# Performance work log

Measured on AMD Instinct MI355X. Metric: run time of the kernel, lower is better.

The kernel has to match this reference:

```python
import jax, jax.numpy as jnp
import numpy as np
from jax.scipy.special import logsumexp

L = 5          # label_size (fixed by label2idx)
START = 3
END = 4
PAD = 2
NEG = -10000.0


def setup_inputs() -> dict:
    B, S = 4096, 512
    key = jax.random.key(0)
    k1, k2, k3, k4 = jax.random.split(key, 4)
    lstm_scores = jax.random.normal(k1, (B, S, L), dtype=jnp.float32)
    transition = jax.random.normal(k2, (L, L), dtype=jnp.float32)
    transition = (transition.at[:, START].set(NEG)
                            .at[END, :].set(NEG)
                            .at[:, PAD].set(NEG)
                            .at[PAD, :].set(NEG))
    word_seq_lens = jax.random.randint(k3, (B,), 1, S + 1)  # lengths in [1, S]
    tags = jax.random.randint(k4, (B, S), 0, 2)             # gold labels in {0,1}
    mask = jnp.arange(S)[None, :] < word_seq_lens[:, None]   # (B, S) bool
    return {"lstm_scores": lstm_scores, "transition": transition,
            "word_seq_lens": word_seq_lens, "tags": tags, "mask": mask}


def reference(lstm_scores, transition, word_seq_lens, tags, mask):
    B, S, _ = lstm_scores.shape
    # all_scores[b,t,i,j] = transition[i,j] + emission[b,t,j]  -> (B,S,L,L)
    all_scores = transition[None, None, :, :] + lstm_scores[:, :, None, :]

    # ---- forward algorithm (normalizer) via scan over time ----
    alpha0 = all_scores[:, 0, START, :]              # (B, L)
    scores_t = jnp.swapaxes(all_scores, 0, 1)        # (S, B, L, L)

    def step(alpha, sc_t):
        new = logsumexp(alpha[:, :, None] + sc_t, axis=1)  # (B, L)
        return new, new

    _, alphas = jax.lax.scan(step, alpha0, scores_t[1:])   # (S-1, B, L)
    alphas = jnp.concatenate([alpha0[None], alphas], axis=0)  # (S, B, L)
    alphas = jnp.swapaxes(alphas, 0, 1)                       # (B, S, L)

    idx = jnp.broadcast_to((word_seq_lens - 1)[:, None, None], (B, 1, L))
    last_alpha = jnp.take_along_axis(alphas, idx, axis=1)[:, 0, :]  # (B, L)
    last_alpha = last_alpha + transition[:, END][None, :]
    unlabeled = jnp.sum(logsumexp(last_alpha, axis=1))

    # ---- gold path score ----
    tag_idx = jnp.broadcast_to(tags[:, :, None, None], (B, S, L, 1))
    cur = jnp.take_along_axis(all_scores, tag_idx, axis=3)[..., 0]  # (B, S, L)
    middle = jnp.take_along_axis(cur[:, 1:, :], tags[:, :-1, None], axis=2)[..., 0]  # (B, S-1)
    begin = cur[:, 0, START]
    end_ids = jnp.take_along_axis(tags, (word_seq_lens - 1)[:, None], axis=1)[:, 0]
    end_sc = transition[end_ids, END]
    labeled = (jnp.sum(begin) + jnp.sum(end_sc)
               + jnp.sum(jnp.where(mask[:, 1:], middle, 0.0)))

    return unlabeled, labeled
```

## Files before the change

kernel.cpp:

```cpp
#include <hip/hip_runtime.h>


#define ROWS 2
#define WPR 2
#define SGS 4

__device__ __forceinline__ void rescale4(float& a, float& b, float& c, float& d,
                                         float& logZ) {
    float m = fmaxf(fmaxf(a, b), fmaxf(c, d));
    int k = (__float_as_int(m) >> 23) & 0xFF;
    float scale = __int_as_float((254 - k) << 23);
    logZ += (float)(k - 127) * 0.69314718055994530942f;
    a *= scale; b *= scale; c *= scale; d *= scale;
}

template <int S>
__global__ __launch_bounds__(64 * ROWS * WPR) void crf_fwd_k1(
    const float* __restrict__ lstm,
    const float* __restrict__ trans,
    const int* __restrict__ lens,
    const int* __restrict__ tags,
    float* __restrict__ ws,
    int B) {
    constexpr int F4R = S * 5 / 4;
    constexpr int T4R = S / 4;
    __shared__ float4 xs4[ROWS][F4R];
    __shared__ int4 tg4[ROWS][T4R];
    __shared__ float cw[ROWS][WPR][6];
    __shared__ float red[2][ROWS];

    const int tid = threadIdx.x;
    const int lane = tid & 63;
    const int w = tid >> 6;
    const int row = w / WPR;
    const int half = w % WPR;
    const int b0 = blockIdx.x * ROWS;

    const int lenA = (b0 < B) ? lens[b0] : 0;
    const int lenB = (b0 + 1 < B) ? lens[b0 + 1] : 0;

    {
        const int nf4_0 = (lenA * 5 + 3) >> 2;
        const int nf4_1 = (lenB * 5 + 3) >> 2;
#pragma unroll
        for (int i = 0; i < (ROWS * F4R) / (64 * ROWS * WPR); ++i) {
            int idx = tid + (64 * ROWS * WPR) * i;
            int r = idx / F4R;
            int j = idx - r * F4R;
            int nf4 = r ? nf4_1 : nf4_0;
            if (j < nf4) {
                const float4* src =
                    reinterpret_cast<const float4*>(lstm + (size_t)(b0 + r) * S * 5);
                xs4[r][j] = src[j];
            }
        }
        const int nt4_0 = (lenA + 3) >> 2;
        const int nt4_1 = (lenB + 3) >> 2;
        {
            int idx = tid;
            if (idx < ROWS * T4R) {
                int r = idx / T4R;
                int j = idx - r * T4R;
                int nt4 = r ? nt4_1 : nt4_0;
                if (j < nt4) {
                    const int4* tsrc =
                        reinterpret_cast<const int4*>(tags + (size_t)(b0 + r) * S);
                    tg4[r][j] = tsrc[j];
                }
            }
        }
    }
    __syncthreads();

    const int b = b0 + row;
    const bool valid = (b < B);
    const int len = row ? lenB : lenA;
    const float* __restrict__ xr = reinterpret_cast<const float*>(xs4[row]);
    const int* __restrict__ tr = reinterpret_cast<const int*>(tg4[row]);

    const float T00 = trans[0], T01 = trans[1];
    const float T04 = trans[4];
    const float T10 = trans[5], T11 = trans[6];
    const float T14 = trans[9];
    const float T30 = trans[15], T31 = trans[16];
    const float E00 = __expf(T00), E01 = __expf(T01);
    const float E10 = __expf(T10), E11 = __expf(T11);

    const int tA = 1 + (half * 64 + lane) * SGS;
    const int tB = min(tA + SGS, len);

    float m00 = 1.f, m01 = 0.f, m10 = 0.f, m11 = 1.f;
    float logZ = 0.f;
    float lab = 0.f;

    if (tA < len) {
        int prev = tr[tA - 1] & 1;
#pragma unroll
        for (int u = 0; u < SGS; ++u) {
            int t = tA + u;
            if (t < tB) {
                float x0 = xr[t * 5 + 0];
                float x1 = xr[t * 5 + 1];
                int tg = tr[t] & 1;
                float ex0 = __expf(x0), ex1 = __expf(x1);
                float n00 = E00 * ex0, n01 = E10 * ex0;
                float n10 = E01 * ex1, n11 = E11 * ex1;
                float r00 = fmaf(n00, m00, n01 * m10);
                float r01 = fmaf(n00, m01, n01 * m11);
                float r10 = fmaf(n10, m00, n11 * m10);
                float r11 = fmaf(n10, m01, n11 * m11);
                m00 = r00; m01 = r01; m10 = r10; m11 = r11;
                int idx = (prev << 1) | tg;
                float Tpt = (idx == 0) ? T00 : (idx == 1) ? T01
                                         : (idx == 2) ? T10 : T11;
                lab += Tpt + (tg ? x1 : x0);
                if (t == len - 1) lab += tg ? T14 : T04;
                prev = tg;
            }
        }
        rescale4(m00, m01, m10, m11, logZ);
    }

#pragma unroll
    for (int msk = 1; msk < 64; msk <<= 1) {
        float o00 = __shfl_xor(m00, msk);
        float o01 = __shfl_xor(m01, msk);
        float o10 = __shfl_xor(m10, msk);
        float o11 = __shfl_xor(m11, msk);
        float oz = __shfl_xor(logZ, msk);
        float ol = __shfl_xor(lab, msk);
        const bool upper = (lane & msk) != 0;
        float a00 = upper ? m00 : o00, a01 = upper ? m01 : o01;
        float a10 = upper ? m10 : o10, a11 = upper ? m11 : o11;
        float c00 = upper ? o00 : m00, c01 = upper ? o01 : m01;
        float c10 = upper ? o10 : m10, c11 = upper ? o11 : m11;
        m00 = fmaf(a00, c00, a01 * c10);
        m01 = fmaf(a00, c01, a01 * c11);
        m10 = fmaf(a10, c00, a11 * c10);
        m11 = fmaf(a10, c01, a11 * c11);
        logZ += oz;
        lab += ol;
        rescale4(m00, m01, m10, m11, logZ);
    }

    if (lane == 0) {
        cw[row][half][0] = m00; cw[row][half][1] = m01;
        cw[row][half][2] = m10; cw[row][half][3] = m11;
        cw[row][half][4] = logZ; cw[row][half][5] = lab;
    }
    __syncthreads();

    if (half == 0 && lane == 0) {
        float unlab_w = 0.f, lab_w = 0.f;
        if (valid) {
            float a00 = cw[row][0][0], a01 = cw[row][0][1];
            float a10 = cw[row][0][2], a11 = cw[row][0][3];
            float b00 = cw[row][1][0], b01 = cw[row][1][1];
            float b10 = cw[row][1][2], b11 = cw[row][1][3];
            float M00 = fmaf(b00, a00, b01 * a10);
            float M01 = fmaf(b00, a01, b01 * a11);
            float M10 = fmaf(b10, a00, b11 * a10);
            float M11 = fmaf(b10, a01, b11 * a11);
            float lz = cw[row][0][4] + cw[row][1][4];
            float lb = cw[row][0][5] + cw[row][1][5];

            float x00 = xr[0], x01 = xr[1];
            int tg0 = tr[0] & 1;
            float p0 = __expf(T30 + x00);
            float p1 = __expf(T31 + x01);
            float f0 = fmaf(M00, p0, M01 * p1);
            float f1 = fmaf(M10, p0, M11 * p1);
            float s = fmaf(f0, __expf(T04), f1 * __expf(T14));
            unlab_w = lz + __logf(s);
            lab_w = lb + (tg0 ? T31 + x01 : T30 + x00);
            if (len == 1) lab_w += tg0 ? T14 : T04;
        }
        red[0][row] = unlab_w;
        red[1][row] = lab_w;
    }
    __syncthreads();
    if (tid == 0) {
        float su = 0.f, sl = 0.f;
#pragma unroll
        for (int r = 0; r < ROWS; ++r) {
            su += red[0][r];
            sl += red[1][r];
        }
        ws[blockIdx.x * 2 + 0] = su;
        ws[blockIdx.x * 2 + 1] = sl;
    }
}

__global__ __launch_bounds__(1024) void crf_reduce(const float* __restrict__ ws,
                                                   float* __restrict__ out,
                                                   int nblk) {
    float su = 0.f, sl = 0.f;
    for (int i = threadIdx.x; i < nblk; i += 1024) {
        float2 v = reinterpret_cast<const float2*>(ws)[i];
        su += v.x;
        sl += v.y;
    }
#pragma unroll
    for (int m = 1; m < 64; m <<= 1) {
        su += __shfl_xor(su, m);
        sl += __shfl_xor(sl, m);
    }
    __shared__ float r[2][16];
    int w = threadIdx.x >> 6, lane = threadIdx.x & 63;
    if (lane == 0) {
        r[0][w] = su;
        r[1][w] = sl;
    }
    __syncthreads();
    if (threadIdx.x == 0) {
        float a = 0.f, b = 0.f;
#pragma unroll
        for (int i = 0; i < 16; ++i) {
            a += r[0][i];
            b += r[1][i];
        }
        out[0] = a;
        out[1] = b;
    }
}

__global__ __launch_bounds__(256) void crf_fwd_wave_gen(
    const float* __restrict__ lstm, const float* __restrict__ trans,
    const int* __restrict__ lens, const int* __restrict__ tags,
    float* __restrict__ out, int B, int S, int Sg) {
    const int lane = threadIdx.x & 63;
    const int wid = threadIdx.x >> 6;
    const int nw = blockDim.x >> 6;
    const int b = blockIdx.x * nw + wid;
    const bool valid = (b < B);

    const float T00 = trans[0], T01 = trans[1];
    const float T04 = trans[4];
    const float T10 = trans[5], T11 = trans[6];
    const float T14 = trans[9];
    const float T30 = trans[15], T31 = trans[16];
    const float E00 = __expf(T00), E01 = __expf(T01);
    const float E10 = __expf(T10), E11 = __expf(T11);

    const int len = valid ? lens[b] : 0;
    const float* __restrict__ xrow = lstm + (size_t)b * S * 5;
    const int* __restrict__ trow = tags + (size_t)b * S;

    const int tA = 1 + lane * Sg;
    const int tB = min(tA + Sg, len);

    float m00 = 1.f, m01 = 0.f, m10 = 0.f, m11 = 1.f;
    float logZ = 0.f, lab = 0.f;

    if (tA < len) {
        int prev = trow[tA - 1] & 1;
        for (int u = 0; u < Sg; ++u) {
            int t = tA + u;
            if (t < tB) {
                float x0 = xrow[t * 5 + 0];
                float x1 = xrow[t * 5 + 1];
                int tg = trow[t] & 1;
                float ex0 = __expf(x0), ex1 = __expf(x1);
                float n00 = E00 * ex0, n01 = E10 * ex0;
                float n10 = E01 * ex1, n11 = E11 * ex1;
                float r00 = fmaf(n00, m00, n01 * m10);
                float r01 = fmaf(n00, m01, n01 * m11);
                float r10 = fmaf(n10, m00, n11 * m10);
                float r11 = fmaf(n10, m01, n11 * m11);
                m00 = r00; m01 = r01; m10 = r10; m11 = r11;
                int idx = (prev << 1) | tg;
                float Tpt = (idx == 0) ? T00 : (idx == 1) ? T01
                                         : (idx == 2) ? T10 : T11;
                lab += Tpt + (tg ? x1 : x0);
                if (t == len - 1) lab += tg ? T14 : T04;
                prev = tg;
            }
            if ((u & 3) == 3) rescale4(m00, m01, m10, m11, logZ);
        }
        rescale4(m00, m01, m10, m11, logZ);
    }

#pragma unroll
    for (int msk = 1; msk < 64; msk <<= 1) {
        float o00 = __shfl_xor(m00, msk);
        float o01 = __shfl_xor(m01, msk);
        float o10 = __shfl_xor(m10, msk);
        float o11 = __shfl_xor(m11, msk);
        float oz = __shfl_xor(logZ, msk);
        float ol = __shfl_xor(lab, msk);
        const bool upper = (lane & msk) != 0;
        float a00 = upper ? m00 : o00, a01 = upper ? m01 : o01;
        float a10 = upper ? m10 : o10, a11 = upper ? m11 : o11;
        float c00 = upper ? o00 : m00, c01 = upper ? o01 : m01;
        float c10 = upper ? o10 : m10, c11 = upper ? o11 : m11;
        m00 = fmaf(a00, c00, a01 * c10);
        m01 = fmaf(a00, c01, a01 * c11);
        m10 = fmaf(a10, c00, a11 * c10);
        m11 = fmaf(a10, c01, a11 * c11);
        logZ += oz;
        lab += ol;
        rescale4(m00, m01, m10, m11, logZ);
    }

    __shared__ float red[2][8];
    float unlab_w = 0.f, lab_w = 0.f;
    if (lane == 0 && valid) {
        float x00 = xrow[0], x01 = xrow[1];
        int tg0 = trow[0] & 1;
        float p0 = __expf(T30 + x00);
        float p1 = __expf(T31 + x01);
        float f0 = fmaf(m00, p0, m01 * p1);
        float f1 = fmaf(m10, p0, m11 * p1);
        float s = fmaf(f0, __expf(T04), f1 * __expf(T14));
        unlab_w = logZ + __logf(s);
        lab_w = lab + (tg0 ? T31 + x01 : T30 + x00);
        if (len == 1) lab_w += tg0 ? T14 : T04;
    }
    if (lane == 0) {
        red[0][wid] = unlab_w;
        red[1][wid] = lab_w;
    }
    __syncthreads();
    if (threadIdx.x == 0) {
        float su = 0.f, sl = 0.f;
        for (int w = 0; w < nw; ++w) {
            su += red[0][w];
            sl += red[1][w];
        }
        atomicAdd(&out[0], su);
        atomicAdd(&out[1], sl);
    }
}

extern "C" void kernel_launch(void* const* d_in, const int* in_sizes, int n_in,
                              void* d_out, int out_size, void* d_ws, size_t ws_size,
                              hipStream_t stream) {
    const float* lstm = (const float*)d_in[0];
    const float* trans = (const float*)d_in[1];
    const int* lens = (const int*)d_in[2];
    const int* tags = (const int*)d_in[3];
    float* out = (float*)d_out;
    float* ws = (float*)d_ws;

    const int B = in_sizes[2];
    const int S = in_sizes[3] / B;

    if (S == 512) {
        const int nblk = (B + ROWS - 1) / ROWS;
        dim3 block(64 * ROWS * WPR);
        crf_fwd_k1<512><<<nblk, block, 0, stream>>>(lstm, trans, lens, tags, ws, B);
        crf_reduce<<<1, 1024, 0, stream>>>(ws, out, nblk);
    } else {
        const int Sg = (S - 1 + 63) >> 6;
        hipMemsetAsync(out, 0, out_size * sizeof(float), stream);
        dim3 block(256);
        dim3 grid((B + 3) / 4);
        crf_fwd_wave_gen<<<grid, block, 0, stream>>>(lstm, trans, lens, tags,
                                                     out, B, S, Sg);
    }
}
```

Before: 99.66 us.

## Fuse final reduction into main kernel via last-block atomic; compact emissions in LDS

Removes the separate reduction kernel launch: each block writes its partial sums, bumps an atomic counter, and the last block to finish reduces all partials and writes the output. A memset of the counter is added before launch. The staging of emissions into shared memory now keeps only the two used label columns per timestep, so the LDS footprint shrinks and the inner loop reads one float2. This trades one kernel launch for a memset plus an atomic and fences per block, and the scatter during staging adds integer divisions.

```diff
diff --git a/kernel.cpp b/kernel.cpp
--- a/kernel.cpp
+++ b/kernel.cpp
@@ -21,13 +21,17 @@
     const int* __restrict__ lens,
     const int* __restrict__ tags,
     float* __restrict__ ws,
+    float* __restrict__ out,
     int B) {
     constexpr int F4R = S * 5 / 4;
     constexpr int T4R = S / 4;
-    __shared__ float4 xs4[ROWS][F4R];
+    constexpr int NTHR = 64 * ROWS * WPR;
+
+    __shared__ float xsc[ROWS][S * 2];
     __shared__ int4 tg4[ROWS][T4R];
     __shared__ float cw[ROWS][WPR][6];
     __shared__ float red[2][ROWS];
+    __shared__ int islast;
 
     const int tid = threadIdx.x;
     const int lane = tid & 63;
@@ -43,15 +47,24 @@
         const int nf4_0 = (lenA * 5 + 3) >> 2;
         const int nf4_1 = (lenB * 5 + 3) >> 2;
 #pragma unroll
-        for (int i = 0; i < (ROWS * F4R) / (64 * ROWS * WPR); ++i) {
-            int idx = tid + (64 * ROWS * WPR) * i;
+        for (int i = 0; i < (ROWS * F4R) / NTHR; ++i) {
+            int idx = tid + NTHR * i;
             int r = idx / F4R;
             int j = idx - r * F4R;
             int nf4 = r ? nf4_1 : nf4_0;
             if (j < nf4) {
                 const float4* src =
                     reinterpret_cast<const float4*>(lstm + (size_t)(b0 + r) * S * 5);
-                xs4[r][j] = src[j];
+                float4 v = src[j];
+                unsigned p0 = 4u * (unsigned)j;
+                float e[4] = {v.x, v.y, v.z, v.w};
+#pragma unroll
+                for (int q = 0; q < 4; ++q) {
+                    unsigned p = p0 + q;
+                    unsigned t = p / 5u;
+                    unsigned c = p - 5u * t;
+                    if (c < 2u) xsc[r][t * 2 + c] = e[q];
+                }
             }
         }
         const int nt4_0 = (lenA + 3) >> 2;
@@ -75,7 +88,7 @@
     const int b = b0 + row;
     const bool valid = (b < B);
     const int len = row ? lenB : lenA;
-    const float* __restrict__ xr = reinterpret_cast<const float*>(xs4[row]);
+    const float2* __restrict__ xr2 = reinterpret_cast<const float2*>(xsc[row]);
     const int* __restrict__ tr = reinterpret_cast<const int*>(tg4[row]);
 
     const float T00 = trans[0], T01 = trans[1];
@@ -99,8 +112,8 @@
         for (int u = 0; u < SGS; ++u) {
             int t = tA + u;
             if (t < tB) {
-                float x0 = xr[t * 5 + 0];
-                float x1 = xr[t * 5 + 1];
+                float2 xv = xr2[t];
+                float x0 = xv.x, x1 = xv.y;
                 int tg = tr[t] & 1;
                 float ex0 = __expf(x0), ex1 = __expf(x1);
                 float n00 = E00 * ex0, n01 = E10 * ex0;
@@ -164,7 +177,7 @@
             float lz = cw[row][0][4] + cw[row][1][4];
             float lb = cw[row][0][5] + cw[row][1][5];
 
-            float x00 = xr[0], x01 = xr[1];
+            float x00 = xsc[row][0], x01 = xsc[row][1];
             int tg0 = tr[0] & 1;
             float p0 = __expf(T30 + x00);
             float p1 = __expf(T31 + x01);
@@ -179,6 +192,9 @@
         red[1][row] = lab_w;
     }
     __syncthreads();
+
+    const int nblk = gridDim.x;
+    unsigned int* cnt = reinterpret_cast<unsigned int*>(ws + (size_t)nblk * 2);
     if (tid == 0) {
         float su = 0.f, sl = 0.f;
 #pragma unroll
@@ -188,39 +204,42 @@
         }
         ws[blockIdx.x * 2 + 0] = su;
         ws[blockIdx.x * 2 + 1] = sl;
-    }
-}
-
-__global__ __launch_bounds__(1024) void crf_reduce(const float* __restrict__ ws,
-                                                   float* __restrict__ out,
-                                                   int nblk) {
-    float su = 0.f, sl = 0.f;
-    for (int i = threadIdx.x; i < nblk; i += 1024) {
-        float2 v = reinterpret_cast<const float2*>(ws)[i];
-        su += v.x;
-        sl += v.y;
-    }
-#pragma unroll
-    for (int m = 1; m < 64; m <<= 1) {
-        su += __shfl_xor(su, m);
-        sl += __shfl_xor(sl, m);
-    }
-    __shared__ float r[2][16];
-    int w = threadIdx.x >> 6, lane = threadIdx.x & 63;
-    if (lane == 0) {
-        r[0][w] = su;
-        r[1][w] = sl;
-    }
-    __syncthreads();
-    if (threadIdx.x == 0) {
-        float a = 0.f, b = 0.f;
-#pragma unroll
-        for (int i = 0; i < 16; ++i) {
-            a += r[0][i];
-            b += r[1][i];
-        }
-        out[0] = a;
-        out[1] = b;
+        __threadfence();
+        unsigned t = atomicAdd(cnt, 1u);
+        islast = (t == (unsigned)nblk - 1u) ? 1 : 0;
+    }
+    __syncthreads();
+
+    if (islast) {
+        __threadfence();
+        float su = 0.f, sl = 0.f;
+        const float2* p = reinterpret_cast<const float2*>(ws);
+        for (int i = tid; i < nblk; i += NTHR) {
+            float2 v = p[i];
+            su += v.x;
+            sl += v.y;
+        }
+#pragma unroll
+        for (int m = 1; m < 64; m <<= 1) {
+            su += __shfl_xor(su, m);
+            sl += __shfl_xor(sl, m);
+        }
+        __shared__ float fr[2][ROWS * WPR];
+        if (lane == 0) {
+            fr[0][w] = su;
+            fr[1][w] = sl;
+        }
+        __syncthreads();
+        if (tid == 0) {
+            float a = 0.f, bsum = 0.f;
+#pragma unroll
+            for (int i = 0; i < ROWS * WPR; ++i) {
+                a += fr[0][i];
+                bsum += fr[1][i];
+            }
+            out[0] = a;
+            out[1] = bsum;
+        }
     }
 }
 
@@ -347,9 +366,11 @@
 
     if (S == 512) {
         const int nblk = (B + ROWS - 1) / ROWS;
+        hipMemsetAsync((char*)d_ws + (size_t)nblk * 2 * sizeof(float), 0,
+                       sizeof(unsigned int), stream);
         dim3 block(64 * ROWS * WPR);
-        crf_fwd_k1<512><<<nblk, block, 0, stream>>>(lstm, trans, lens, tags, ws, B);
-        crf_reduce<<<1, 1024, 0, stream>>>(ws, out, nblk);
+        crf_fwd_k1<512><<<nblk, block, 0, stream>>>(lstm, trans, lens, tags,
+                                                    ws, out, B);
     } else {
         const int Sg = (S - 1 + 63) >> 6;
         hipMemsetAsync(out, 0, out_size * sizeof(float), stream);
```

Measured after the change: 138.5 us. 39.0% more time.
